# Kernel optimization log

Measured on AMD Instinct MI355X. Metric: run time of the kernel, lower is better.

The kernel has to match this reference:

```python
import jax, jax.numpy as jnp
import numpy as np

B, S, D = 4, 2048, 1024
E, TOP_K = 8, 2
CAPACITY_FACTOR = 1.1
H = 4 * D  # expert hidden dim


def setup_inputs() -> dict:
    key = jax.random.key(0)
    ks = jax.random.split(key, 12)
    sc = 0.02
    return {
        "x": jax.random.normal(ks[0], (B, S, D), jnp.float32),
        "noise": jax.random.normal(ks[1], (B, S, E), jnp.float32),
        "W_route": jax.random.normal(ks[2], (D, E), jnp.float32) * sc,
        "b_route": jnp.zeros((E,), jnp.float32),
        "W_noise": jax.random.normal(ks[3], (D, E), jnp.float32) * sc,
        "b_noise": jnp.zeros((E,), jnp.float32),
        "W1": jax.random.normal(ks[4], (E, D, H), jnp.float32) * sc,
        "b1": jnp.zeros((E, H), jnp.float32),
        "W2": jax.random.normal(ks[5], (E, H, D), jnp.float32) * sc,
        "b2": jnp.zeros((E, D), jnp.float32),
    }


def reference(x, noise, W_route, b_route, W_noise, b_noise, W1, b1, W2, b2):
    # ---- NoisyTopkRouter ----
    logits = x @ W_route + b_route                  # [B,S,E]
    noise_logits = x @ W_noise + b_noise            # [B,S,E]
    noisy = logits + noise * jax.nn.softplus(noise_logits)
    top_vals, top_idx = jax.lax.top_k(noisy, TOP_K)  # [B,S,k]
    probs_k = jax.nn.softmax(top_vals, axis=-1)      # softmax over sparse(-inf elsewhere) == softmax over top-k
    onehot = jax.nn.one_hot(top_idx, E, dtype=x.dtype)          # [B,S,k,E]
    router_probs = jnp.einsum('bske,bsk->bse', onehot, probs_k)  # [B,S,E]
    expert_mask = onehot.sum(axis=-2)                            # [B,S,E] (top_k indices are distinct)
    lb_loss = E * jnp.sum(router_probs.mean(axis=(0, 1)) * expert_mask.mean(axis=(0, 1)))

    # ---- capacity-limited dispatch / expert MLP / combine ----
    T = B * S
    cap = int(T * TOP_K / E * CAPACITY_FACTOR)
    flat_x = x.reshape(T, D)
    flat_gate = router_probs.reshape(T, E)
    mask = expert_mask.reshape(T, E) > 0                         # token selects expert
    pos = jnp.cumsum(mask.astype(jnp.int32), axis=0)             # 1-based slot within expert
    keep = mask & (pos <= cap)                                   # first `cap` tokens per expert (flat order)
    priority = jnp.where(keep, jnp.arange(T)[:, None], T)        # [T,E]
    order = jnp.argsort(priority, axis=0)[:cap]                  # [cap,E] token ids (stable: token order)
    valid = (jnp.take_along_axis(priority, order, axis=0) < T).T  # [E,cap]
    gather_idx = order.T                                         # [E,cap]

    x_e = flat_x[gather_idx]                                     # [E,cap,D]
    h = jax.nn.relu(jnp.einsum('ecd,edh->ech', x_e, W1) + b1[:, None, :])
    out_e = jnp.einsum('ech,ehd->ecd', h, W2) + b2[:, None, :]   # dropout is identity in eval mode
    gate = flat_gate[gather_idx, jnp.arange(E)[:, None]]         # [E,cap]
    weighted = out_e * (gate * valid)[..., None]
    updates = jnp.zeros_like(flat_x).at[gather_idx.reshape(-1)].add(weighted.reshape(-1, D))
    return updates.reshape(B, S, D), lb_loss
```

## Files before the change

### kernel.cpp

```cpp
#include <hip/hip_runtime.h>
#include <hip/hip_bf16.h>

#define D_DIM 1024
#define H_DIM 4096
#define E_NUM 8
#define T_TOK 8192
#define CAPN 2252
#define CAP_PAD 2304
#define MT 9
#define NG1 2304

typedef __attribute__((ext_vector_type(8))) short short8;
typedef __attribute__((ext_vector_type(4))) float f32x4;
typedef __attribute__((ext_vector_type(4))) float f4v;
typedef __attribute__((ext_vector_type(4))) ushort u16x4;
typedef const __attribute__((address_space(1))) void* gas_ptr;
typedef __attribute__((address_space(3))) void* las_ptr;

__device__ __forceinline__ unsigned short f2bf(float f) {
    __hip_bfloat16 h = __float2bfloat16(f);
    return __builtin_bit_cast(unsigned short, h);
}
__device__ __forceinline__ float bfu2f(ushort u) {
    unsigned v = (unsigned)u << 16;
    return __builtin_bit_cast(float, v);
}

__global__ void router_kernel(const float* __restrict__ x,
                              const float* __restrict__ noise,
                              const float* __restrict__ Wr,
                              const float* __restrict__ br,
                              const float* __restrict__ Wn,
                              const float* __restrict__ bn,
                              __hip_bfloat16* __restrict__ xb,
                              int* __restrict__ tok_e,
                              float* __restrict__ tok_g)
{
    const int l = threadIdx.x & 63;
    const int w = threadIdx.x >> 6;
    const int t = blockIdx.x * 4 + w;
    const float* xr = x + (size_t)t * D_DIM;

    float ar[8] = {0,0,0,0,0,0,0,0};
    float an[8] = {0,0,0,0,0,0,0,0};
#pragma unroll
    for (int i = 0; i < 4; ++i) {
        int d = i * 256 + l * 4;
        f4v xv = __builtin_nontemporal_load((const f4v*)(xr + d));
        ushort4 xq;
        xq.x = f2bf(xv.x); xq.y = f2bf(xv.y); xq.z = f2bf(xv.z); xq.w = f2bf(xv.w);
        *(ushort4*)(xb + (size_t)t * D_DIM + d) = xq;
        float xs[4] = {xv.x, xv.y, xv.z, xv.w};
#pragma unroll
        for (int j = 0; j < 4; ++j) {
            const float* wrp = Wr + (size_t)(d + j) * 8;
            float4 wa = *(const float4*)wrp;
            float4 wb = *(const float4*)(wrp + 4);
            ar[0] = fmaf(xs[j], wa.x, ar[0]); ar[1] = fmaf(xs[j], wa.y, ar[1]);
            ar[2] = fmaf(xs[j], wa.z, ar[2]); ar[3] = fmaf(xs[j], wa.w, ar[3]);
            ar[4] = fmaf(xs[j], wb.x, ar[4]); ar[5] = fmaf(xs[j], wb.y, ar[5]);
            ar[6] = fmaf(xs[j], wb.z, ar[6]); ar[7] = fmaf(xs[j], wb.w, ar[7]);
            const float* wnp = Wn + (size_t)(d + j) * 8;
            float4 na = *(const float4*)wnp;
            float4 nb = *(const float4*)(wnp + 4);
            an[0] = fmaf(xs[j], na.x, an[0]); an[1] = fmaf(xs[j], na.y, an[1]);
            an[2] = fmaf(xs[j], na.z, an[2]); an[3] = fmaf(xs[j], na.w, an[3]);
            an[4] = fmaf(xs[j], nb.x, an[4]); an[5] = fmaf(xs[j], nb.y, an[5]);
            an[6] = fmaf(xs[j], nb.z, an[6]); an[7] = fmaf(xs[j], nb.w, an[7]);
        }
    }
#pragma unroll
    for (int e = 0; e < 8; ++e) {
#pragma unroll
        for (int s = 32; s > 0; s >>= 1) {
            ar[e] += __shfl_xor(ar[e], s, 64);
            an[e] += __shfl_xor(an[e], s, 64);
        }
    }
    if (l == 0) {
        float nv[8];
#pragma unroll
        for (int e = 0; e < 8; ++e) {
            float z = an[e] + bn[e];
            float sp = fmaxf(z, 0.f) + log1pf(expf(-fabsf(z)));
            nv[e] = ar[e] + br[e] + noise[(size_t)t * 8 + e] * sp;
        }
        int e0 = 0; float v0 = nv[0];
#pragma unroll
        for (int e = 1; e < 8; ++e) if (nv[e] > v0) { v0 = nv[e]; e0 = e; }
        int e1 = -1; float v1 = -3.4e38f;
#pragma unroll
        for (int e = 0; e < 8; ++e) if (e != e0 && nv[e] > v1) { v1 = nv[e]; e1 = e; }
        float ex = expf(v1 - v0);
        float p0 = 1.f / (1.f + ex);
        float p1 = ex * p0;
        tok_e[2 * t]     = e0; tok_e[2 * t + 1] = e1;
        tok_g[2 * t]     = p0; tok_g[2 * t + 1] = p1;
    }
}

__global__ void scan_kernel(const int* __restrict__ tok_e,
                            const float* __restrict__ tok_g,
                            int* __restrict__ routed,
                            int* __restrict__ inv,
                            int* __restrict__ nkept,
                            float* __restrict__ lb_out)
{
    const int e = threadIdx.x >> 6;
    const int l = threadIdx.x & 63;
    __shared__ float s_g[E_NUM];
    __shared__ int   s_c[E_NUM];

    int run = 0;
    float gsum = 0.f;
    for (int b = 0; b < 8; ++b) {
        int2  ev[16];
        float2 gv[16];
#pragma unroll
        for (int c = 0; c < 16; ++c) {
            int t = (b * 16 + c) * 64 + l;
            ev[c] = ((const int2*)tok_e)[t];
            gv[c] = ((const float2*)tok_g)[t];
        }
#pragma unroll
        for (int c = 0; c < 16; ++c) {
            int t = (b * 16 + c) * 64 + l;
            int j = (ev[c].x == e) ? 0 : ((ev[c].y == e) ? 1 : -1);
            bool sel = (j >= 0);
            unsigned long long m = __ballot(sel);
            if (sel) {
                int pos = run + __popcll(m & ((1ull << l) - 1ull));
                if (pos < CAPN) {
                    routed[e * CAP_PAD + pos] = t;
                    inv[2 * t + j] = e * CAP_PAD + pos;
                }
                gsum += (j == 0) ? gv[c].x : gv[c].y;
            }
            run += __popcll(m);
        }
    }
#pragma unroll
    for (int s = 32; s > 0; s >>= 1) gsum += __shfl_xor(gsum, s, 64);
    int nk = min(run, CAPN);
    for (int s = nk + l; s < CAP_PAD; s += 64) routed[e * CAP_PAD + s] = 0;
    if (l == 0) { nkept[e] = nk; s_g[e] = gsum; s_c[e] = run; }
    __syncthreads();
    if (threadIdx.x == 0) {
        float lb = 0.f;
        for (int ee = 0; ee < E_NUM; ++ee)
            lb += (s_g[ee] / (float)T_TOK) * ((float)s_c[ee] / (float)T_TOK);
        lb_out[0] = lb * (float)E_NUM;
    }
}

__global__ void gather_kernel(const ushort* __restrict__ xb,
                              const int* __restrict__ routed,
                              ushort* __restrict__ xg)
{
    const int dc = blockIdx.x & 127;
    const int e  = blockIdx.x >> 7;
    ushort* dst = xg + (size_t)(e * 128 + dc) * CAP_PAD * 8;
    const int* rte = routed + e * CAP_PAD;
#pragma unroll
    for (int p = 0; p < 9; ++p) {
        int m = p * 256 + threadIdx.x;
        int tok = rte[m];
        ulonglong2 v = *(const ulonglong2*)(xb + (size_t)tok * D_DIM + dc * 8);
        *(ulonglong2*)(dst + (size_t)m * 8) = v;
    }
}

__device__ __forceinline__ void chunk_body(const float* __restrict__ src0,
                                           ushort* __restrict__ dstb,
                                           int K, int N, unsigned i,
                                           float (*tile)[65])
{
    const int nx = N >> 6;
    const int bx = i % nx;
    const unsigned rem = i / nx;
    const int by = rem % (K >> 6);
    const int e  = rem / (K >> 6);
    const int k0 = by * 64, n0 = bx * 64;
    const float* src = src0 + (size_t)e * K * N;
    ushort* dst = dstb + (size_t)e * (K / 8) * N * 8;
    const int t = threadIdx.x;
    const int rr = t >> 4, c4 = (t & 15) * 4;
#pragma unroll
    for (int p = 0; p < 4; ++p) {
        int r = p * 16 + rr;
        f4v v = __builtin_nontemporal_load(
            (const f4v*)(src + (size_t)(k0 + r) * N + n0 + c4));
        tile[r][c4]     = v.x; tile[r][c4 + 1] = v.y;
        tile[r][c4 + 2] = v.z; tile[r][c4 + 3] = v.w;
    }
    __syncthreads();
    const int n = t & 63, kc = t >> 6;
#pragma unroll
    for (int p = 0; p < 2; ++p) {
        int kcc = p * 4 + kc;
        ushort g[8];
#pragma unroll
        for (int j = 0; j < 8; ++j) g[j] = f2bf(tile[kcc * 8 + j][n]);
        *(short8*)(dst + ((size_t)(k0 / 8 + kcc) * N + n0 + n) * 8) = *(const short8*)g;
    }
}

__global__ void chunk_weights(const float* __restrict__ in,
                              ushort* __restrict__ out, int K, int N)
{
    __shared__ float tile[64][65];
    chunk_body(in, out, K, N, blockIdx.x, tile);
}

__global__ __launch_bounds__(256, 2) void gemm1_chunk2(
    const ushort* __restrict__ A,
    const ushort* __restrict__ Bt,
    const float* __restrict__ bias,
    const int* __restrict__ nkept,
    ushort* __restrict__ outH,
    const float* __restrict__ W2,
    ushort* __restrict__ w2c)
{
    __shared__ ushort lds[36864];
    const unsigned blk = blockIdx.x;

    if (blk >= NG1) {
        chunk_body(W2, w2c, H_DIM, D_DIM, blk - NG1, (float(*)[65])lds);
        return;
    }

    constexpr int ND = H_DIM;
    constexpr int NC = D_DIM / 8;
    constexpr int nkt = D_DIM / 32;

    unsigned sw = (blk & 7) * (NG1 >> 3) + (blk >> 3);
    unsigned bn = sw % (H_DIM / 128);
    unsigned t1 = sw / (H_DIM / 128);
    unsigned bm = t1 % MT;
    unsigned e  = t1 / MT;

    const int m0 = (int)bm * 256, n0 = (int)bn * 128;
    if (m0 >= nkept[e]) return;

    const int tid  = threadIdx.x;
    const int lane = tid & 63;
    const int w    = tid >> 6;
    const int aw   = w << 10;
    const int bci  = tid >> 7;
    const int bw   = (w & 1) << 10;

    const size_t sAc = (size_t)CAP_PAD * 8;
    const size_t sBc = (size_t)ND * 8;
    const size_t tsA = 4 * sAc;
    const size_t tsB = 4 * sBc;

    const ushort* Ae = A  + ((size_t)e * NC * CAP_PAD + (size_t)(m0 + tid)) * 8;
    const ushort* Be = Bt + ((size_t)e * NC * ND + (size_t)(n0 + (tid & 127))) * 8
                          + (size_t)bci * sBc;

    auto gl = [&](const ushort* g, int ldsbyte) {
        __builtin_amdgcn_global_load_lds((gas_ptr)g, (las_ptr)((char*)lds + ldsbyte), 16, 0, 0);
    };
    auto issueA = [&](size_t off, int stB) {
        gl(Ae + off,           stB + 0 * 4096 + aw);
        gl(Ae + off + sAc,     stB + 1 * 4096 + aw);
        gl(Ae + off + 2 * sAc, stB + 2 * 4096 + aw);
        gl(Ae + off + 3 * sAc, stB + 3 * 4096 + aw);
    };
    auto issueB = [&](size_t off, int stB) {
        gl(Be + off,           stB + 16384 + (0 + bci) * 2048 + bw);
        gl(Be + off + 2 * sBc, stB + 16384 + (2 + bci) * 2048 + bw);
    };

    issueA(0, 0);        issueB(0, 0);
    issueA(tsA, 24576);  issueB(tsB, 24576);
    asm volatile("s_waitcnt vmcnt(6)" ::: "memory");
    __builtin_amdgcn_s_barrier();

    f32x4 acc[8][4] = {};
    const int wm = (w >> 1) * 128;
    const int wn = (w & 1) * 64;
    const int fr = lane & 15;
    const int fq = lane >> 4;

    int rdS = 0;
    int wrB = 49152;
    size_t oA = 2 * tsA;
    size_t oB = 2 * tsB;

    for (int kt = 0; kt < nkt; ++kt) {
        const ushort* Ard = lds + rdS;
        const ushort* Brd = lds + rdS + 8192;

        short8 af[8], bfr[4];
#pragma unroll
        for (int j = 0; j < 4; ++j)
            bfr[j] = *(const short8*)(Brd + fq * 1024 + (wn + j * 16 + fr) * 8);
#pragma unroll
        for (int i = 0; i < 8; ++i)
            af[i] = *(const short8*)(Ard + fq * 2048 + (wm + i * 16 + fr) * 8);

        issueA(oA, wrB);
        issueB(oB, wrB);

        __builtin_amdgcn_s_setprio(1);
#pragma unroll
        for (int i = 0; i < 8; ++i)
#pragma unroll
            for (int j = 0; j < 4; ++j)
                acc[i][j] = __builtin_amdgcn_mfma_f32_16x16x32_bf16(af[i], bfr[j], acc[i][j], 0, 0, 0);
        __builtin_amdgcn_s_setprio(0);

        asm volatile("s_waitcnt vmcnt(6)" ::: "memory");
        __builtin_amdgcn_s_barrier();

        rdS = (rdS == 24576) ? 0 : rdS + 12288;
        wrB = (wrB == 49152) ? 0 : wrB + 24576;
        if (kt < nkt - 3) { oA += tsA; oB += tsB; }
    }

#pragma unroll
    for (int j = 0; j < 4; ++j) {
        int nc = n0 + wn + j * 16 + fr;
        float bv = bias[e * ND + nc];
#pragma unroll
        for (int i = 0; i < 8; ++i) {
            int mr = m0 + wm + i * 16 + (fq << 2);
#pragma unroll
            for (int r = 0; r < 4; ++r) {
                float v = fmaxf(acc[i][j][r] + bv, 0.f);
                outH[(((size_t)e * 512 + (nc >> 3)) * CAP_PAD + mr + r) * 8 + (nc & 7)] = f2bf(v);
            }
        }
    }
}

__global__ __launch_bounds__(256, 2) void ffn_gemm2(
    const ushort* __restrict__ A,
    const ushort* __restrict__ Bt,
    const int* __restrict__ nkept,
    ushort* __restrict__ outP,
    int sshift, int nkt)
{
    constexpr int KD = H_DIM;
    constexpr int ND = D_DIM;
    constexpr int NC = KD / 8;
    __shared__ ushort lds[36864];

    unsigned total = gridDim.x * gridDim.y * gridDim.z;
    unsigned flat  = blockIdx.x + gridDim.x * (blockIdx.y + gridDim.y * blockIdx.z);
    unsigned sw    = (flat & 7) * (total >> 3) + (flat >> 3);
    unsigned bn    = sw % gridDim.x;
    unsigned t1    = sw / gridDim.x;
    unsigned bm    = t1 % gridDim.y;
    unsigned bz    = t1 / gridDim.y;

    const int e  = (int)(bz >> sshift);
    const int sp = (int)(bz & ((1u << sshift) - 1u));
    const int m0 = (int)bm * 256, n0 = (int)bn * 128;
    if (m0 >= nkept[e]) return;
    const int kc0 = sp * (nkt << 2);

    const int tid  = threadIdx.x;
    const int lane = tid & 63;
    const int w    = tid >> 6;
    const int aw   = w << 10;
    const int bci  = tid >> 7;
    const int bw   = (w & 1) << 10;

    const size_t sAc = (size_t)CAP_PAD * 8;
    const size_t sBc = (size_t)ND * 8;
    const size_t tsA = 4 * sAc;
    const size_t tsB = 4 * sBc;

    const ushort* Ae = A  + ((size_t)e * NC * CAP_PAD + (size_t)(m0 + tid)) * 8
                          + (size_t)kc0 * sAc;
    const ushort* Be = Bt + ((size_t)e * NC * ND + (size_t)(n0 + (tid & 127))) * 8
                          + (size_t)(kc0 + bci) * sBc;

    auto gl = [&](const ushort* g, int ldsbyte) {
        __builtin_amdgcn_global_load_lds((gas_ptr)g, (las_ptr)((char*)lds + ldsbyte), 16, 0, 0);
    };
    auto issueA = [&](size_t off, int stB) {
        gl(Ae + off,           stB + 0 * 4096 + aw);
        gl(Ae + off + sAc,     stB + 1 * 4096 + aw);
        gl(Ae + off + 2 * sAc, stB + 2 * 4096 + aw);
        gl(Ae + off + 3 * sAc, stB + 3 * 4096 + aw);
    };
    auto issueB = [&](size_t off, int stB) {
        gl(Be + off,           stB + 16384 + (0 + bci) * 2048 + bw);
        gl(Be + off + 2 * sBc, stB + 16384 + (2 + bci) * 2048 + bw);
    };

    issueA(0, 0);        issueB(0, 0);
    issueA(tsA, 24576);  issueB(tsB, 24576);
    asm volatile("s_waitcnt vmcnt(6)" ::: "memory");
    __builtin_amdgcn_s_barrier();

    f32x4 acc[8][4] = {};
    const int wm = (w >> 1) * 128;
    const int wn = (w & 1) * 64;
    const int fr = lane & 15;
    const int fq = lane >> 4;

    int rdS = 0;
    int wrB = 49152;
    size_t oA = 2 * tsA;
    size_t oB = 2 * tsB;

    for (int kt = 0; kt < nkt; ++kt) {
        const ushort* Ard = lds + rdS;
        const ushort* Brd = lds + rdS + 8192;

        short8 af[8], bfr[4];
#pragma unroll
        for (int j = 0; j < 4; ++j)
            bfr[j] = *(const short8*)(Brd + fq * 1024 + (wn + j * 16 + fr) * 8);
#pragma unroll
        for (int i = 0; i < 8; ++i)
            af[i] = *(const short8*)(Ard + fq * 2048 + (wm + i * 16 + fr) * 8);

        issueA(oA, wrB);
        issueB(oB, wrB);

        __builtin_amdgcn_s_setprio(1);
#pragma unroll
        for (int i = 0; i < 8; ++i)
#pragma unroll
            for (int j = 0; j < 4; ++j)
                acc[i][j] = __builtin_amdgcn_mfma_f32_16x16x32_bf16(af[i], bfr[j], acc[i][j], 0, 0, 0);
        __builtin_amdgcn_s_setprio(0);

        asm volatile("s_waitcnt vmcnt(6)" ::: "memory");
        __builtin_amdgcn_s_barrier();

        rdS = (rdS == 24576) ? 0 : rdS + 12288;
        wrB = (wrB == 49152) ? 0 : wrB + 24576;
        if (kt < nkt - 3) { oA += tsA; oB += tsB; }
    }

#pragma unroll
    for (int j = 0; j < 4; ++j) {
        int nc = n0 + wn + j * 16 + fr;
#pragma unroll
        for (int i = 0; i < 8; ++i) {
            int mr = m0 + wm + i * 16 + (fq << 2);
#pragma unroll
            for (int r = 0; r < 4; ++r)
                outP[((size_t)(sp * E_NUM + e) * CAP_PAD + mr + r) * D_DIM + nc] =
                    f2bf(acc[i][j][r]);
        }
    }
}

__global__ void combine_kernel(const ushort* __restrict__ part,
                               const int* __restrict__ inv,
                               const float* __restrict__ tok_g,
                               const float* __restrict__ b2,
                               int S,
                               float* __restrict__ out)
{
    const int t = blockIdx.x;
    const int d = threadIdx.x * 4;
    f4v r = {0.f, 0.f, 0.f, 0.f};
#pragma unroll
    for (int j = 0; j < 2; ++j) {
        int i = inv[2 * t + j];
        if (i >= 0) {
            float g = tok_g[2 * t + j];
            int e = i / CAP_PAD;
            f4v a = *(const f4v*)(b2 + (size_t)e * D_DIM + d);
            for (int s = 0; s < S; ++s) {
                u16x4 p = __builtin_nontemporal_load(
                    (const u16x4*)(part + ((size_t)s * E_NUM * CAP_PAD + i) * D_DIM + d));
                a.x += bfu2f(p.x); a.y += bfu2f(p.y);
                a.z += bfu2f(p.z); a.w += bfu2f(p.w);
            }
            r += g * a;
        }
    }
    __builtin_nontemporal_store(r, (f4v*)(out + (size_t)t * D_DIM + d));
}

extern "C" void kernel_launch(void* const* d_in, const int* in_sizes, int n_in,
                              void* d_out, int out_size, void* d_ws, size_t ws_size,
                              hipStream_t stream)
{
    const float* x  = (const float*)d_in[0];
    const float* nz = (const float*)d_in[1];
    const float* Wr = (const float*)d_in[2];
    const float* br = (const float*)d_in[3];
    const float* Wn = (const float*)d_in[4];
    const float* bn = (const float*)d_in[5];
    const float* W1 = (const float*)d_in[6];
    const float* b1 = (const float*)d_in[7];
    const float* W2 = (const float*)d_in[8];
    const float* b2 = (const float*)d_in[9];
    float* out = (float*)d_out;
    char* ws = (char*)d_ws;

    const size_t sz_w2c = (size_t)E_NUM * (H_DIM / 8) * D_DIM * 8 * 2;
    const size_t sz_h   = (size_t)E_NUM * 512 * CAP_PAD * 8 * 2;
    const size_t o_w2c  = 0;
    const size_t o_h    = o_w2c + sz_w2c;
    const size_t o_sm   = o_h + sz_h;
    const size_t o_dyn  = o_sm + (1u << 20);
    const size_t sz_xg  = (size_t)E_NUM * 128 * CAP_PAD * 8 * 2;
    const size_t sz_xb  = (size_t)T_TOK * D_DIM * 2;
    const size_t sz_w1c = (size_t)E_NUM * (D_DIM / 8) * H_DIM * 8 * 2;
    const size_t sz_p1  = sz_xg + sz_xb + sz_w1c;
    const size_t sz_part1 = (size_t)E_NUM * CAP_PAD * D_DIM * 2;

    int sshift = 1;
    while (sshift > 0) {
        size_t need = o_dyn + ((sz_part1 << sshift) > sz_p1 ? (sz_part1 << sshift) : sz_p1);
        if (need <= ws_size) break;
        --sshift;
    }
    const int S = 1 << sshift;

    ushort* w2c  = (ushort*)(ws + o_w2c);
    ushort* hbuf = (ushort*)(ws + o_h);
    int*    rt   = (int*)(ws + o_sm);
    int*    te   = (int*)(ws + o_sm + 131072);
    float*  tg   = (float*)(ws + o_sm + 262144);
    int*    inv  = (int*)(ws + o_sm + 393216);
    int*    nk   = (int*)(ws + o_sm + 524288);
    ushort* xg   = (ushort*)(ws + o_dyn);
    ushort* xb   = (ushort*)(ws + o_dyn + sz_xg);
    ushort* w1c  = (ushort*)(ws + o_dyn + sz_xg + sz_xb);
    ushort* part = (ushort*)(ws + o_dyn);

    (void)hipMemsetAsync(inv, 0xFF, (size_t)T_TOK * 2 * 4, stream);

    router_kernel<<<T_TOK / 4, 256, 0, stream>>>(x, nz, Wr, br, Wn, bn,
                                                 (__hip_bfloat16*)xb, te, tg);
    scan_kernel<<<1, 512, 0, stream>>>(te, tg, rt, inv, nk, out + (size_t)T_TOK * D_DIM);
    chunk_weights<<<(H_DIM / 64) * (D_DIM / 64) * E_NUM, 256, 0, stream>>>(W1, w1c, D_DIM, H_DIM);
    gather_kernel<<<E_NUM * 128, 256, 0, stream>>>(xb, rt, xg);

    gemm1_chunk2<<<NG1 + (D_DIM / 64) * (H_DIM / 64) * E_NUM, 256, 0, stream>>>(
        xg, w1c, b1, nk, hbuf, W2, w2c);

    ffn_gemm2<<<dim3(D_DIM / 128, MT, E_NUM << sshift), 256, 0, stream>>>(
        hbuf, w2c, nk, part, sshift, (H_DIM / 32) >> sshift);

    combine_kernel<<<T_TOK, 256, 0, stream>>>(part, inv, tg, b2, S, out);
}
```

Before: 532.0 us.

## Rewrite weight chunking without LDS, fuse W1 chunking into gather, drop memset

The fp32-to-bf16 weight repacking now reads 8 rows of 4 floats per thread straight from registers and writes packed 8-element k-chunks, instead of staging a 64x64 tile in shared memory with a barrier. W1 conversion is merged into the gather kernel's launch, removing one kernel launch. The memset of the inverse map is replaced by having the scan kernel write -1 for tokens dropped by capacity. This trades the tile transpose for strided per-thread loads and wider blocks, and relies on the scan covering every (token, k) slot.

Result: no change. 528.4 us (-0.7%).

```diff
diff --git a/kernel.cpp b/kernel.cpp
--- a/kernel.cpp
+++ b/kernel.cpp
@@ -24,6 +24,32 @@
 __device__ __forceinline__ float bfu2f(ushort u) {
     unsigned v = (unsigned)u << 16;
     return __builtin_bit_cast(float, v);
+}
+
+__device__ __forceinline__ void chunk_body(const float* __restrict__ src0,
+                                           ushort* __restrict__ dstb,
+                                           int K, int N, unsigned i)
+{
+    const int nkc = K >> 3;
+    const int kc  = i % nkc;
+    const unsigned rem = i / nkc;
+    const int nn  = N >> 10;
+    const int n0  = (int)(rem % nn) << 10;
+    const int e   = (int)(rem / nn);
+    const int nt  = n0 + threadIdx.x * 4;
+    const float* src = src0 + (size_t)e * K * N + (size_t)(kc * 8) * N + nt;
+    ushort* dst = dstb + (size_t)e * (K / 8) * N * 8 + ((size_t)kc * N + nt) * 8;
+    f4v v[8];
+#pragma unroll
+    for (int j = 0; j < 8; ++j)
+        v[j] = __builtin_nontemporal_load((const f4v*)(src + (size_t)j * N));
+#pragma unroll
+    for (int d = 0; d < 4; ++d) {
+        ushort g[8];
+#pragma unroll
+        for (int j = 0; j < 8; ++j) g[j] = f2bf(v[j][d]);
+        *(short8*)(dst + (size_t)d * 8) = *(const short8*)g;
+    }
 }
 
 __global__ void router_kernel(const float* __restrict__ x,
@@ -133,6 +159,8 @@
                 if (pos < CAPN) {
                     routed[e * CAP_PAD + pos] = t;
                     inv[2 * t + j] = e * CAP_PAD + pos;
+                } else {
+                    inv[2 * t + j] = -1;
                 }
                 gsum += (j == 0) ? gv[c].x : gv[c].y;
             }
@@ -153,12 +181,20 @@
     }
 }
 
-__global__ void gather_kernel(const ushort* __restrict__ xb,
-                              const int* __restrict__ routed,
-                              ushort* __restrict__ xg)
-{
-    const int dc = blockIdx.x & 127;
-    const int e  = blockIdx.x >> 7;
+__global__ __launch_bounds__(256) void gather_chunk1(
+    const ushort* __restrict__ xb,
+    const int* __restrict__ routed,
+    ushort* __restrict__ xg,
+    const float* __restrict__ W1,
+    ushort* __restrict__ w1c)
+{
+    const unsigned blk = blockIdx.x;
+    if (blk >= 1024) {
+        chunk_body(W1, w1c, D_DIM, H_DIM, blk - 1024);
+        return;
+    }
+    const int dc = blk & 127;
+    const int e  = blk >> 7;
     ushort* dst = xg + (size_t)(e * 128 + dc) * CAP_PAD * 8;
     const int* rte = routed + e * CAP_PAD;
 #pragma unroll
@@ -168,48 +204,6 @@
         ulonglong2 v = *(const ulonglong2*)(xb + (size_t)tok * D_DIM + dc * 8);
         *(ulonglong2*)(dst + (size_t)m * 8) = v;
     }
-}
-
-__device__ __forceinline__ void chunk_body(const float* __restrict__ src0,
-                                           ushort* __restrict__ dstb,
-                                           int K, int N, unsigned i,
-                                           float (*tile)[65])
-{
-    const int nx = N >> 6;
-    const int bx = i % nx;
-    const unsigned rem = i / nx;
-    const int by = rem % (K >> 6);
-    const int e  = rem / (K >> 6);
-    const int k0 = by * 64, n0 = bx * 64;
-    const float* src = src0 + (size_t)e * K * N;
-    ushort* dst = dstb + (size_t)e * (K / 8) * N * 8;
-    const int t = threadIdx.x;
-    const int rr = t >> 4, c4 = (t & 15) * 4;
-#pragma unroll
-    for (int p = 0; p < 4; ++p) {
-        int r = p * 16 + rr;
-        f4v v = __builtin_nontemporal_load(
-            (const f4v*)(src + (size_t)(k0 + r) * N + n0 + c4));
-        tile[r][c4]     = v.x; tile[r][c4 + 1] = v.y;
-        tile[r][c4 + 2] = v.z; tile[r][c4 + 3] = v.w;
-    }
-    __syncthreads();
-    const int n = t & 63, kc = t >> 6;
-#pragma unroll
-    for (int p = 0; p < 2; ++p) {
-        int kcc = p * 4 + kc;
-        ushort g[8];
-#pragma unroll
-        for (int j = 0; j < 8; ++j) g[j] = f2bf(tile[kcc * 8 + j][n]);
-        *(short8*)(dst + ((size_t)(k0 / 8 + kcc) * N + n0 + n) * 8) = *(const short8*)g;
-    }
-}
-
-__global__ void chunk_weights(const float* __restrict__ in,
-                              ushort* __restrict__ out, int K, int N)
-{
-    __shared__ float tile[64][65];
-    chunk_body(in, out, K, N, blockIdx.x, tile);
 }
 
 __global__ __launch_bounds__(256, 2) void gemm1_chunk2(
@@ -225,7 +219,7 @@
     const unsigned blk = blockIdx.x;
 
     if (blk >= NG1) {
-        chunk_body(W2, w2c, H_DIM, D_DIM, blk - NG1, (float(*)[65])lds);
+        chunk_body(W2, w2c, H_DIM, D_DIM, blk - NG1);
         return;
     }
 
@@ -531,15 +525,14 @@
     ushort* w1c  = (ushort*)(ws + o_dyn + sz_xg + sz_xb);
     ushort* part = (ushort*)(ws + o_dyn);
 
-    (void)hipMemsetAsync(inv, 0xFF, (size_t)T_TOK * 2 * 4, stream);
-
     router_kernel<<<T_TOK / 4, 256, 0, stream>>>(x, nz, Wr, br, Wn, bn,
                                                  (__hip_bfloat16*)xb, te, tg);
     scan_kernel<<<1, 512, 0, stream>>>(te, tg, rt, inv, nk, out + (size_t)T_TOK * D_DIM);
-    chunk_weights<<<(H_DIM / 64) * (D_DIM / 64) * E_NUM, 256, 0, stream>>>(W1, w1c, D_DIM, H_DIM);
-    gather_kernel<<<E_NUM * 128, 256, 0, stream>>>(xb, rt, xg);
-
-    gemm1_chunk2<<<NG1 + (D_DIM / 64) * (H_DIM / 64) * E_NUM, 256, 0, stream>>>(
+
+    gather_chunk1<<<1024 + (D_DIM / 8) * (H_DIM / 1024) * E_NUM, 256, 0, stream>>>(
+        xb, rt, xg, W1, w1c);
+
+    gemm1_chunk2<<<NG1 + (H_DIM / 8) * (D_DIM / 1024) * E_NUM, 256, 0, stream>>>(
         xg, w1c, b1, nk, hbuf, W2, w2c);
 
     ffn_gemm2<<<dim3(D_DIM / 128, MT, E_NUM << sshift), 256, 0, stream>>>(
```
